# Optimization experiments

Measured on AMD Instinct MI355X. Metric: run time of the kernel, lower is better.

Reference implementation:

```python
import jax, jax.numpy as jnp
import numpy as np

D_IN = 1024
D_OUT = 1024
NUM_HEADS = 16
HEAD_DIM = D_OUT // NUM_HEADS
CONTEXT_LEN = 2048


def setup_inputs() -> dict:
    key = jax.random.key(0)
    ks = jax.random.split(key, 7)
    scale = 0.02
    x = jax.random.normal(ks[0], (2, 2048, D_IN), dtype=jnp.float32)
    Wq = jax.random.normal(ks[1], (D_IN, D_OUT), dtype=jnp.float32) * scale
    bq = jnp.zeros((D_OUT,), dtype=jnp.float32)
    Wk = jax.random.normal(ks[2], (D_IN, D_OUT), dtype=jnp.float32) * scale
    bk = jnp.zeros((D_OUT,), dtype=jnp.float32)
    Wv = jax.random.normal(ks[3], (D_IN, D_OUT), dtype=jnp.float32) * scale
    bv = jnp.zeros((D_OUT,), dtype=jnp.float32)
    return {"x": x, "Wq": Wq, "bq": bq, "Wk": Wk, "bk": bk, "Wv": Wv, "bv": bv}


def reference(x, Wq, bq, Wk, bk, Wv, bv):
    B, S, _ = x.shape
    # QKV projections with bias
    q = x @ Wq + bq  # [B,S,D_OUT]
    k = x @ Wk + bk
    v = x @ Wv + bv
    # split heads -> [B,H,S,Dh]
    def heads(t):
        return t.reshape(B, S, NUM_HEADS, HEAD_DIM).transpose(0, 2, 1, 3)
    q, k, v = heads(q), heads(k), heads(v)
    # raw scores, then additive causal mask (-1e9 on strictly upper triangle),
    # then scale by 1/sqrt(head_dim) AFTER adding mask (matches original code)
    scores = jnp.einsum("bhqd,bhkd->bhqk", q, k)
    causal = jnp.tril(jnp.ones((S, S), dtype=bool))
    add_mask = jnp.where(causal, 0.0, -1e9).astype(scores.dtype)
    scores = scores + add_mask
    weights = jax.nn.softmax(scores / jnp.sqrt(jnp.asarray(HEAD_DIM, scores.dtype)), axis=-1)
    ctx = jnp.einsum("bhqk,bhkd->bhqd", weights, v)  # [B,H,S,Dh]
    return ctx.transpose(0, 2, 1, 3).reshape(B, S, D_OUT)
```

## Files before the change

kernel.cpp:

```cpp
#include <hip/hip_runtime.h>
#include <hip/hip_bf16.h>
#include <stdint.h>

#define D_IN 1024
#define NH 16
#define DH 64
#define SEQ 2048
#define BATCH 2

typedef unsigned short u16;
typedef __attribute__((ext_vector_type(8))) short short8;
typedef __attribute__((ext_vector_type(4))) float f32x4;

#define CSCALE 0.1803368801f

__device__ __forceinline__ u16 f2bf(float f) {
    union { float f; uint32_t u; } v; v.f = f;
    uint32_t r = v.u + 0x7FFF + ((v.u >> 16) & 1);
    return (u16)(r >> 16);
}

__device__ __forceinline__ float bf2f(u16 u) {
    union { uint32_t u; float f; } v; v.u = (uint32_t)u << 16;
    return v.f;
}

__device__ __forceinline__ uint32_t pktrunc(float a, float b) {
    union { float f; uint32_t u; } x, y;
    x.f = a; y.f = b;
    return __builtin_amdgcn_perm(y.u, x.u, 0x07060302u);
}

__device__ __forceinline__ void async16(const u16* g, u16* l) {
    __builtin_amdgcn_global_load_lds(
        (const __attribute__((address_space(1))) void*)g,
        (__attribute__((address_space(3))) void*)l, 16, 0, 0);
}

__global__ __launch_bounds__(256) void prep_kernel(
    const float* __restrict__ x, const float* __restrict__ Wq,
    const float* __restrict__ Wk, const float* __restrict__ Wv,
    u16* __restrict__ xb, u16* __restrict__ WT)
{
    __shared__ float tile[64][65];
    if (blockIdx.x < 4096) {
        int i = (blockIdx.x * 256 + threadIdx.x) * 4;
        float4 v = *(const float4*)(x + i);
        union { u16 u[4]; uint2 d; } o;
        o.u[0] = f2bf(v.x); o.u[1] = f2bf(v.y); o.u[2] = f2bf(v.z); o.u[3] = f2bf(v.w);
        *(uint2*)(xb + i) = o.d;
        return;
    }
    int idx = blockIdx.x - 4096;
    int mat = idx >> 8, rem = idx & 255;
    int k0 = (rem & 15) * 64, n0 = (rem >> 4) * 64;
    const float* W = (mat == 0) ? Wq : (mat == 1 ? Wk : Wv);
    int c = threadIdx.x & 63, rb = threadIdx.x >> 6;
    #pragma unroll
    for (int p = 0; p < 16; ++p) {
        int r = p * 4 + rb;
        tile[r][c] = W[(size_t)(k0 + r) * 1024 + n0 + c];
    }
    __syncthreads();
    #pragma unroll
    for (int p = 0; p < 16; ++p) {
        int r = p * 4 + rb;
        WT[((size_t)mat * 1024 + n0 + r) * 1024 + k0 + c] = f2bf(tile[c][r]);
    }
}

__global__ __launch_bounds__(512, 2) void qkv_gemm_kernel(
    const u16* __restrict__ xb, const u16* __restrict__ WT,
    const float* __restrict__ bq, const float* __restrict__ bk,
    const float* __restrict__ bv,
    u16* __restrict__ Qb, u16* __restrict__ Kb, u16* __restrict__ Vt)
{
    __shared__ u16 smem[65536];
    u16* As = smem;
    u16* Bs = smem + 32768;

    const int tid  = threadIdx.x;
    const int wave = tid >> 6, lane = tid & 63;
    const int quad = lane >> 4, l15 = lane & 15;
    const int wm = wave >> 2, wn = wave & 3;
    const int fsig = l15 & 7;

    const int lin = blockIdx.x;
    const int logical = (lin & 7) * 24 + (lin >> 3);
    const int by = logical / 12;
    const int bx = logical % 12;
    const int m0 = by * 256;
    const int n0 = bx * 256;

    const int ch  = tid & 7;
    const int rwT = tid >> 3;

    f32x4 acc[8][4];
    #pragma unroll
    for (int i = 0; i < 8; ++i)
        #pragma unroll
        for (int j = 0; j < 4; ++j)
            acc[i][j] = (f32x4){0.f, 0.f, 0.f, 0.f};

    auto stageA = [&](int buf, int kst) {
        #pragma unroll
        for (int r = 0; r < 4; ++r) {
            int row = r * 64 + rwT;
            int g = ch ^ (row & 7);
            async16(xb + (size_t)(m0 + row) * 1024 + kst + g * 8,
                    As + buf * 16384 + row * 64 + ch * 8);
        }
    };
    auto stageBh = [&](int buf, int kst, int half) {
        #pragma unroll
        for (int r = 0; r < 2; ++r) {
            int row = half * 128 + r * 64 + rwT;
            int g = ch ^ (row & 7);
            async16(WT + (size_t)(n0 + row) * 1024 + kst + g * 8,
                    Bs + buf * 16384 + row * 64 + ch * 8);
        }
    };

    stageA(0, 0);  stageBh(0, 0, 0);  stageBh(0, 0, 1);
    stageA(1, 64); stageBh(1, 64, 0); stageBh(1, 64, 1);
    asm volatile("s_waitcnt vmcnt(8)" ::: "memory");
    __builtin_amdgcn_sched_barrier(0);
    __builtin_amdgcn_s_barrier();

    for (int t = 0; t < 16; ++t) {
        const int cur = t & 1;
        const u16* Ab = As + cur * 16384;
        const u16* Bb = Bs + cur * 16384;
        const bool st = (t + 2 < 16);
        const int k2 = (t + 2) * 64;

        short8 bfr[4][2];
        #pragma unroll
        for (int j = 0; j < 4; ++j)
            #pragma unroll
            for (int kk = 0; kk < 2; ++kk)
                bfr[j][kk] = *(const short8*)(Bb + (wn * 64 + j * 16 + l15) * 64 +
                                              (((kk << 2) + quad) ^ fsig) * 8);

        #pragma unroll
        for (int p = 0; p < 4; ++p) {
            short8 af[2][2];
            #pragma unroll
            for (int i2 = 0; i2 < 2; ++i2)
                #pragma unroll
                for (int kk = 0; kk < 2; ++kk)
                    af[i2][kk] = *(const short8*)(Ab + (wm * 128 + (p * 2 + i2) * 16 + l15) * 64 +
                                                  (((kk << 2) + quad) ^ fsig) * 8);
            if (p == 1 && st) stageBh(cur, k2, 0);
            if (p == 2 && st) stageBh(cur, k2, 1);
            __builtin_amdgcn_s_barrier();
            if (p == 3 && st) stageA(cur, k2);
            __builtin_amdgcn_s_setprio(1);
            #pragma unroll
            for (int kk = 0; kk < 2; ++kk)
                #pragma unroll
                for (int i2 = 0; i2 < 2; ++i2)
                    #pragma unroll
                    for (int j = 0; j < 4; ++j)
                        acc[p * 2 + i2][j] = __builtin_amdgcn_mfma_f32_16x16x32_bf16(
                            af[i2][kk], bfr[j][kk], acc[p * 2 + i2][j], 0, 0, 0);
            __builtin_amdgcn_s_setprio(0);
            if (p == 3) {
                if (st)            { asm volatile("s_waitcnt vmcnt(8)" ::: "memory"); }
                else if (t == 14)  { asm volatile("s_waitcnt vmcnt(0)" ::: "memory"); }
                __builtin_amdgcn_sched_barrier(0);
            }
            __builtin_amdgcn_s_barrier();
        }
    }
    __syncthreads();

    const int mat = n0 >> 10;
    const int ncb = (n0 & 1023) + wn * 64;
    const int hh = ncb >> 6;
    const int bb = m0 >> 11, sb = m0 & 2047;

    if (mat < 2) {
        const float* bias = (mat == 0) ? bq : bk;
        u16* dst = (mat == 0) ? Qb : Kb;
        const float sc = (mat == 0) ? CSCALE : 1.0f;
        #pragma unroll
        for (int i = 0; i < 8; ++i) {
            int ss = sb + wm * 128 + i * 16 + quad * 4;
            #pragma unroll
            for (int j = 0; j < 4; ++j) {
                int dh = j * 16 + l15;
                float bval = bias[ncb + dh];
                size_t base = (((size_t)bb * NH + hh) * SEQ + ss) * DH + dh;
                #pragma unroll
                for (int r = 0; r < 4; ++r)
                    dst[base + (size_t)r * DH] = f2bf((acc[i][j][r] + bval) * sc);
            }
        }
    } else {
        u16* vt = smem + wave * (64 * 72);
        u16* vdst = Vt + ((size_t)(bb * NH + hh) * DH) * SEQ;
        #pragma unroll
        for (int h2 = 0; h2 < 2; ++h2) {
            #pragma unroll
            for (int i = 0; i < 4; ++i)
                #pragma unroll
                for (int j = 0; j < 4; ++j) {
                    float bval = bv[ncb + j * 16 + l15];
                    union { u16 u[4]; uint2 d; } o;
                    #pragma unroll
                    for (int r = 0; r < 4; ++r)
                        o.u[r] = f2bf(acc[h2 * 4 + i][j][r] + bval);
                    *(uint2*)(vt + (j * 16 + l15) * 72 + i * 16 + quad * 4) = o.d;
                }
            const int s0w = sb + wm * 128 + h2 * 64;
            #pragma unroll
            for (int it = 0; it < 8; ++it) {
                int dh = it * 8 + (lane >> 3);
                short8 v = *(const short8*)(vt + dh * 72 + (lane & 7) * 8);
                *(short8*)(vdst + (size_t)dh * SEQ + s0w + (lane & 7) * 8) = v;
            }
        }
    }
}

__device__ __forceinline__ void stage64(const u16* g0, size_t gstride, u16* lds,
                                        int wave, int lane)
{
    #pragma unroll
    for (int rnd = 0; rnd < 2; ++rnd) {
        int row = rnd * 32 + wave * 8 + (lane >> 3);
        int sig = ((row >> 3) & 1) * 4 + (row & 3);
        int c = (lane & 7) ^ sig;
        async16(g0 + (size_t)row * gstride + c * 8, lds + row * 64 + (lane & 7) * 8);
    }
}

__global__ __launch_bounds__(256) void flash_mfma_kernel(
    const u16* __restrict__ Qb, const u16* __restrict__ Kb,
    const u16* __restrict__ Vt, float* __restrict__ out,
    u16* __restrict__ Opart, float* __restrict__ Lpart)
{
    static const int JQT[24] = {7,15,15,14,14, 6,13,13,12,12, 5,11,11,10,10,
                                4, 9, 9, 8, 8, 3, 2, 1, 0};
    static const int JHF[24] = {-1,0,1,0,1, -1,0,1,0,1, -1,0,1,0,1,
                                -1,0,1,0,1, -1,-1,-1,-1};

    __shared__ u16 Ks[3][64 * 64];
    __shared__ u16 Vs[3][64 * 64];

    const int tid  = threadIdx.x;
    const int wave = tid >> 6, lane = tid & 63;
    const int quad = lane >> 4, l15 = lane & 15;
    const int bhx = blockIdx.x;
    const int b = bhx >> 4, h = bhx & 15;
    const int job = blockIdx.y;
    const int qt = JQT[job], hf = JHF[job];
    const int t0 = (hf == 1) ? qt + 1 : 0;
    const int t1 = (hf == 0) ? qt + 1 : 2 * qt + 2;
    const int q0 = qt * 128;
    const int wq0 = wave * 32;
    const size_t bh = (size_t)bhx;
    const u16* Qp = Qb + bh * SEQ * DH;
    const u16* Kp = Kb + bh * SEQ * DH;
    const u16* Vp = Vt + bh * DH * SEQ;

    short8 qf[2][2];
    #pragma unroll
    for (int qa = 0; qa < 2; ++qa) {
        const u16* qrp = Qp + (size_t)(q0 + wq0 + qa * 16 + l15) * DH;
        qf[qa][0] = *(const short8*)(qrp + quad * 8);
        qf[qa][1] = *(const short8*)(qrp + 32 + quad * 8);
    }

    const short8 ones = (short8){0x3F80, 0x3F80, 0x3F80, 0x3F80,
                                 0x3F80, 0x3F80, 0x3F80, 0x3F80};

    f32x4 O[2][4], L[2];
    #pragma unroll
    for (int pa = 0; pa < 2; ++pa) {
        #pragma unroll
        for (int f = 0; f < 4; ++f) O[pa][f] = (f32x4){0.f, 0.f, 0.f, 0.f};
        L[pa] = (f32x4){0.f, 0.f, 0.f, 0.f};
    }

    const int wqmax = q0 + wq0 + 31;
    const int krbase = (l15 >> 2) * 8 + (l15 & 3);
    const int ksig   = ((l15 >> 2) & 1) * 4 + (l15 & 3);
    const int vsig   = ((l15 >> 3) & 1) * 4 + (l15 & 3);

    int cur = t0 % 3;
    stage64(Kp + (size_t)t0 * 64 * DH, DH, Ks[cur], wave, lane);
    stage64(Vp + t0 * 64, SEQ, Vs[cur], wave, lane);
    if (t0 + 1 < t1) {
        int nb = cur + 1; if (nb >= 3) nb -= 3;
        stage64(Kp + (size_t)(t0 + 1) * 64 * DH, DH, Ks[nb], wave, lane);
        stage64(Vp + (t0 + 1) * 64, SEQ, Vs[nb], wave, lane);
        asm volatile("s_waitcnt vmcnt(4)" ::: "memory");
    } else {
        asm volatile("s_waitcnt vmcnt(0)" ::: "memory");
    }
    __builtin_amdgcn_sched_barrier(0);
    __builtin_amdgcn_s_barrier();

    for (int t = t0; t < t1; ++t) {
        const bool st = (t + 2 < t1);
        if (st) {
            int s2 = cur + 2; if (s2 >= 3) s2 -= 3;
            int k2 = (t + 2) * 64;
            stage64(Kp + (size_t)k2 * DH, DH, Ks[s2], wave, lane);
            stage64(Vp + k2, SEQ, Vs[s2], wave, lane);
        }
        const int k0 = t * 64;
        if (k0 <= wqmax) {
            f32x4 sf[4][2];
            __builtin_amdgcn_s_setprio(1);
            #pragma unroll
            for (int fj = 0; fj < 4; ++fj) {
                int krow = (fj >> 1) * 32 + krbase + (fj & 1) * 4;
                const u16* kp = &Ks[cur][krow * 64];
                short8 k0f = *(const short8*)(kp + (quad ^ ksig) * 8);
                short8 k1f = *(const short8*)(kp + ((4 + quad) ^ ksig) * 8);
                #pragma unroll
                for (int qa = 0; qa < 2; ++qa) {
                    f32x4 s = (f32x4){0.f, 0.f, 0.f, 0.f};
                    s = __builtin_amdgcn_mfma_f32_16x16x32_bf16(k0f, qf[qa][0], s, 0, 0, 0);
                    s = __builtin_amdgcn_mfma_f32_16x16x32_bf16(k1f, qf[qa][1], s, 0, 0, 0);
                    sf[fj][qa] = s;
                }
            }
            __builtin_amdgcn_s_setprio(0);
            const bool diag = (k0 + 63 > q0 + wq0);
            short8 pA[2][2];
            #pragma unroll
            for (int qa = 0; qa < 2; ++qa) {
                #pragma unroll
                for (int fj = 0; fj < 4; ++fj)
                    #pragma unroll
                    for (int r = 0; r < 4; ++r) {
                        float p = __builtin_amdgcn_exp2f(sf[fj][qa][r]);
                        if (diag) {
                            int key = k0 + (fj >> 1) * 32 + quad * 8 + (fj & 1) * 4 + r;
                            int qg  = q0 + wq0 + qa * 16 + l15;
                            p = (key <= qg) ? p : 0.f;
                        }
                        sf[fj][qa][r] = p;
                    }
                union { uint32_t d[4]; short8 v; } a0, a1;
                a0.d[0] = pktrunc(sf[0][qa][0], sf[0][qa][1]);
                a0.d[1] = pktrunc(sf[0][qa][2], sf[0][qa][3]);
                a0.d[2] = pktrunc(sf[1][qa][0], sf[1][qa][1]);
                a0.d[3] = pktrunc(sf[1][qa][2], sf[1][qa][3]);
                a1.d[0] = pktrunc(sf[2][qa][0], sf[2][qa][1]);
                a1.d[1] = pktrunc(sf[2][qa][2], sf[2][qa][3]);
                a1.d[2] = pktrunc(sf[3][qa][0], sf[3][qa][1]);
                a1.d[3] = pktrunc(sf[3][qa][2], sf[3][qa][3]);
                pA[qa][0] = a0.v;
                pA[qa][1] = a1.v;
                L[qa] = __builtin_amdgcn_mfma_f32_16x16x32_bf16(pA[qa][0], ones, L[qa], 0, 0, 0);
                L[qa] = __builtin_amdgcn_mfma_f32_16x16x32_bf16(pA[qa][1], ones, L[qa], 0, 0, 0);
            }
            __builtin_amdgcn_s_setprio(1);
            #pragma unroll
            for (int fo = 0; fo < 4; ++fo) {
                const u16* vrow = &Vs[cur][(fo * 16 + l15) * 64];
                short8 vb0 = *(const short8*)(vrow + (quad ^ vsig) * 8);
                short8 vb1 = *(const short8*)(vrow + ((4 + quad) ^ vsig) * 8);
                #pragma unroll
                for (int pa = 0; pa < 2; ++pa) {
                    O[pa][fo] = __builtin_amdgcn_mfma_f32_16x16x32_bf16(pA[pa][0], vb0, O[pa][fo], 0, 0, 0);
                    O[pa][fo] = __builtin_amdgcn_mfma_f32_16x16x32_bf16(pA[pa][1], vb1, O[pa][fo], 0, 0, 0);
                }
            }
            __builtin_amdgcn_s_setprio(0);
        }
        if (t + 1 < t1) {
            if (st) { asm volatile("s_waitcnt vmcnt(4)" ::: "memory"); }
            else    { asm volatile("s_waitcnt vmcnt(0)" ::: "memory"); }
            __builtin_amdgcn_sched_barrier(0);
            __builtin_amdgcn_s_barrier();
        }
        cur = (cur + 1 >= 3) ? 0 : cur + 1;
    }

    if (hf < 0) {
        #pragma unroll
        for (int pa = 0; pa < 2; ++pa)
            #pragma unroll
            for (int fo = 0; fo < 4; ++fo)
                #pragma unroll
                for (int r = 0; r < 4; ++r) {
                    int s = q0 + wq0 + pa * 16 + quad * 4 + r;
                    out[((size_t)b * SEQ + s) * 1024 + h * DH + fo * 16 + l15] =
                        O[pa][fo][r] / L[pa][r];
                }
    } else {
        const int pi = (qt - 8) * 2 + hf;
        u16* op = Opart + (((size_t)pi * 32 + bhx) * 128) * 64;
        float* lp = Lpart + ((size_t)pi * 32 + bhx) * 128;
        #pragma unroll
        for (int pa = 0; pa < 2; ++pa) {
            #pragma unroll
            for (int fo = 0; fo < 4; ++fo)
                #pragma unroll
                for (int r = 0; r < 4; ++r) {
                    int ql = wq0 + pa * 16 + quad * 4 + r;
                    op[(size_t)ql * 64 + fo * 16 + l15] = f2bf(O[pa][fo][r]);
                }
            if (l15 == 0) {
                #pragma unroll
                for (int r = 0; r < 4; ++r)
                    lp[wq0 + pa * 16 + quad * 4 + r] = L[pa][r];
            }
        }
    }
}

__global__ __launch_bounds__(256) void combine_kernel(
    const u16* __restrict__ Opart, const float* __restrict__ Lpart,
    float* __restrict__ out)
{
    int blk = blockIdx.x;
    int qt = 8 + (blk >> 5);
    int bh = blk & 31;
    int b = bh >> 4, h = bh & 15;
    int pi0 = (qt - 8) * 2, pi1 = pi0 + 1;
    int tid = threadIdx.x;
    int q = tid >> 1, seg = (tid & 1) * 32;
    const u16* o0 = Opart + (((size_t)pi0 * 32 + bh) * 128 + q) * 64 + seg;
    const u16* o1 = Opart + (((size_t)pi1 * 32 + bh) * 128 + q) * 64 + seg;
    float inv = 1.0f / (Lpart[((size_t)pi0 * 32 + bh) * 128 + q] +
                        Lpart[((size_t)pi1 * 32 + bh) * 128 + q]);
    float* op = out + ((size_t)b * SEQ + qt * 128 + q) * 1024 + h * DH + seg;
    #pragma unroll
    for (int d = 0; d < 32; d += 4) {
        union { uint2 d2; u16 u[4]; } a, c;
        a.d2 = *(const uint2*)(o0 + d);
        c.d2 = *(const uint2*)(o1 + d);
        float4 v;
        v.x = (bf2f(a.u[0]) + bf2f(c.u[0])) * inv;
        v.y = (bf2f(a.u[1]) + bf2f(c.u[1])) * inv;
        v.z = (bf2f(a.u[2]) + bf2f(c.u[2])) * inv;
        v.w = (bf2f(a.u[3]) + bf2f(c.u[3])) * inv;
        *(float4*)(op + d) = v;
    }
}

extern "C" void kernel_launch(void* const* d_in, const int* in_sizes, int n_in,
                              void* d_out, int out_size, void* d_ws, size_t ws_size,
                              hipStream_t stream) {
    const float* x  = (const float*)d_in[0];
    const float* Wq = (const float*)d_in[1];
    const float* bq = (const float*)d_in[2];
    const float* Wk = (const float*)d_in[3];
    const float* bk = (const float*)d_in[4];
    const float* Wv = (const float*)d_in[5];
    const float* bv = (const float*)d_in[6];
    float* out = (float*)d_out;

    const size_t NX = (size_t)BATCH * SEQ * D_IN;
    const size_t NW = (size_t)3 * D_IN * 1024;
    const size_t NP = (size_t)BATCH * NH * SEQ * DH;
    u16* xb = (u16*)d_ws;
    u16* WT = xb + NX;
    u16* Qb = WT + NW;
    u16* Kb = Qb + NP;
    u16* Vt = Kb + NP;
    u16* Opart = xb;
    float* Lpart = (float*)(xb + NX);

    prep_kernel<<<4096 + 768, 256, 0, stream>>>(x, Wq, Wk, Wv, xb, WT);
    qkv_gemm_kernel<<<dim3(192), 512, 0, stream>>>(xb, WT, bq, bk, bv, Qb, Kb, Vt);
    flash_mfma_kernel<<<dim3(32, 24), 256, 0, stream>>>(Qb, Kb, Vt, out, Opart, Lpart);
    combine_kernel<<<256, 256, 0, stream>>>(Opart, Lpart, out);
}
```

Baseline: 156.2 us.

## Drop split-KV work partitioning and combine kernel; one block per query tile

Removes the split-K scheme where long query tiles (8-15) were divided into two halves written as bf16 partials and merged by a separate combine kernel. Each block now processes a full 128-row query tile over all its causal key tiles, with the longest tiles scheduled first, and writes normalized output directly. This saves a kernel launch, the partial-result round trip through memory and the bf16 rounding of partials. In exchange the grid shrinks from 768 to 512 blocks and per-block work becomes more unbalanced, which can leave a long tail on the longest tiles.

```diff
diff --git a/kernel.cpp b/kernel.cpp
--- a/kernel.cpp
+++ b/kernel.cpp
@@ -238,13 +238,9 @@
 
 __global__ __launch_bounds__(256) void flash_mfma_kernel(
     const u16* __restrict__ Qb, const u16* __restrict__ Kb,
-    const u16* __restrict__ Vt, float* __restrict__ out,
-    u16* __restrict__ Opart, float* __restrict__ Lpart)
+    const u16* __restrict__ Vt, float* __restrict__ out)
 {
-    static const int JQT[24] = {7,15,15,14,14, 6,13,13,12,12, 5,11,11,10,10,
-                                4, 9, 9, 8, 8, 3, 2, 1, 0};
-    static const int JHF[24] = {-1,0,1,0,1, -1,0,1,0,1, -1,0,1,0,1,
-                                -1,0,1,0,1, -1,-1,-1,-1};
+    static const int QT[16] = {15,14,13,12,11,10,9,8, 0,1,2,3,4,5,6,7};
 
     __shared__ u16 Ks[3][64 * 64];
     __shared__ u16 Vs[3][64 * 64];
@@ -254,10 +250,8 @@
     const int quad = lane >> 4, l15 = lane & 15;
     const int bhx = blockIdx.x;
     const int b = bhx >> 4, h = bhx & 15;
-    const int job = blockIdx.y;
-    const int qt = JQT[job], hf = JHF[job];
-    const int t0 = (hf == 1) ? qt + 1 : 0;
-    const int t1 = (hf == 0) ? qt + 1 : 2 * qt + 2;
+    const int qt = QT[blockIdx.y];
+    const int t1 = 2 * qt + 2;
     const int q0 = qt * 128;
     const int wq0 = wave * 32;
     const size_t bh = (size_t)bhx;
@@ -289,21 +283,16 @@
     const int ksig   = ((l15 >> 2) & 1) * 4 + (l15 & 3);
     const int vsig   = ((l15 >> 3) & 1) * 4 + (l15 & 3);
 
-    int cur = t0 % 3;
-    stage64(Kp + (size_t)t0 * 64 * DH, DH, Ks[cur], wave, lane);
-    stage64(Vp + t0 * 64, SEQ, Vs[cur], wave, lane);
-    if (t0 + 1 < t1) {
-        int nb = cur + 1; if (nb >= 3) nb -= 3;
-        stage64(Kp + (size_t)(t0 + 1) * 64 * DH, DH, Ks[nb], wave, lane);
-        stage64(Vp + (t0 + 1) * 64, SEQ, Vs[nb], wave, lane);
-        asm volatile("s_waitcnt vmcnt(4)" ::: "memory");
-    } else {
-        asm volatile("s_waitcnt vmcnt(0)" ::: "memory");
-    }
+    int cur = 0;
+    stage64(Kp, DH, Ks[0], wave, lane);
+    stage64(Vp, SEQ, Vs[0], wave, lane);
+    stage64(Kp + (size_t)64 * DH, DH, Ks[1], wave, lane);
+    stage64(Vp + 64, SEQ, Vs[1], wave, lane);
+    asm volatile("s_waitcnt vmcnt(4)" ::: "memory");
     __builtin_amdgcn_sched_barrier(0);
     __builtin_amdgcn_s_barrier();
 
-    for (int t = t0; t < t1; ++t) {
+    for (int t = 0; t < t1; ++t) {
         const bool st = (t + 2 < t1);
         if (st) {
             int s2 = cur + 2; if (s2 >= 3) s2 -= 3;
@@ -383,67 +372,16 @@
         cur = (cur + 1 >= 3) ? 0 : cur + 1;
     }
 
-    if (hf < 0) {
-        #pragma unroll
-        for (int pa = 0; pa < 2; ++pa)
-            #pragma unroll
-            for (int fo = 0; fo < 4; ++fo)
-                #pragma unroll
-                for (int r = 0; r < 4; ++r) {
-                    int s = q0 + wq0 + pa * 16 + quad * 4 + r;
-                    out[((size_t)b * SEQ + s) * 1024 + h * DH + fo * 16 + l15] =
-                        O[pa][fo][r] / L[pa][r];
-                }
-    } else {
-        const int pi = (qt - 8) * 2 + hf;
-        u16* op = Opart + (((size_t)pi * 32 + bhx) * 128) * 64;
-        float* lp = Lpart + ((size_t)pi * 32 + bhx) * 128;
-        #pragma unroll
-        for (int pa = 0; pa < 2; ++pa) {
-            #pragma unroll
-            for (int fo = 0; fo < 4; ++fo)
-                #pragma unroll
-                for (int r = 0; r < 4; ++r) {
-                    int ql = wq0 + pa * 16 + quad * 4 + r;
-                    op[(size_t)ql * 64 + fo * 16 + l15] = f2bf(O[pa][fo][r]);
-                }
-            if (l15 == 0) {
-                #pragma unroll
-                for (int r = 0; r < 4; ++r)
-                    lp[wq0 + pa * 16 + quad * 4 + r] = L[pa][r];
-            }
-        }
-    }
-}
-
-__global__ __launch_bounds__(256) void combine_kernel(
-    const u16* __restrict__ Opart, const float* __restrict__ Lpart,
-    float* __restrict__ out)
-{
-    int blk = blockIdx.x;
-    int qt = 8 + (blk >> 5);
-    int bh = blk & 31;
-    int b = bh >> 4, h = bh & 15;
-    int pi0 = (qt - 8) * 2, pi1 = pi0 + 1;
-    int tid = threadIdx.x;
-    int q = tid >> 1, seg = (tid & 1) * 32;
-    const u16* o0 = Opart + (((size_t)pi0 * 32 + bh) * 128 + q) * 64 + seg;
-    const u16* o1 = Opart + (((size_t)pi1 * 32 + bh) * 128 + q) * 64 + seg;
-    float inv = 1.0f / (Lpart[((size_t)pi0 * 32 + bh) * 128 + q] +
-                        Lpart[((size_t)pi1 * 32 + bh) * 128 + q]);
-    float* op = out + ((size_t)b * SEQ + qt * 128 + q) * 1024 + h * DH + seg;
-    #pragma unroll
-    for (int d = 0; d < 32; d += 4) {
-        union { uint2 d2; u16 u[4]; } a, c;
-        a.d2 = *(const uint2*)(o0 + d);
-        c.d2 = *(const uint2*)(o1 + d);
-        float4 v;
-        v.x = (bf2f(a.u[0]) + bf2f(c.u[0])) * inv;
-        v.y = (bf2f(a.u[1]) + bf2f(c.u[1])) * inv;
-        v.z = (bf2f(a.u[2]) + bf2f(c.u[2])) * inv;
-        v.w = (bf2f(a.u[3]) + bf2f(c.u[3])) * inv;
-        *(float4*)(op + d) = v;
-    }
+    #pragma unroll
+    for (int pa = 0; pa < 2; ++pa)
+        #pragma unroll
+        for (int fo = 0; fo < 4; ++fo)
+            #pragma unroll
+            for (int r = 0; r < 4; ++r) {
+                int s = q0 + wq0 + pa * 16 + quad * 4 + r;
+                out[((size_t)b * SEQ + s) * 1024 + h * DH + fo * 16 + l15] =
+                    O[pa][fo][r] / L[pa][r];
+            }
 }
 
 extern "C" void kernel_launch(void* const* d_in, const int* in_sizes, int n_in,
@@ -466,11 +404,8 @@
     u16* Qb = WT + NW;
     u16* Kb = Qb + NP;
     u16* Vt = Kb + NP;
-    u16* Opart = xb;
-    float* Lpart = (float*)(xb + NX);
 
     prep_kernel<<<4096 + 768, 256, 0, stream>>>(x, Wq, Wk, Wv, xb, WT);
     qkv_gemm_kernel<<<dim3(192), 512, 0, stream>>>(xb, WT, bq, bk, bv, Qb, Kb, Vt);
-    flash_mfma_kernel<<<dim3(32, 24), 256, 0, stream>>>(Qb, Kb, Vt, out, Opart, Lpart);
-    combine_kernel<<<256, 256, 0, stream>>>(Opart, Lpart, out);
-}
+    flash_mfma_kernel<<<dim3(32, 16), 256, 0, stream>>>(Qb, Kb, Vt, out);
+}
```

New measurement: 166.7 us. +6.7%, slower.
